# Optimization experiments

Hardware: AMD Instinct MI355X
Metric: run time of the kernel (lower is better)

## Reference

```python
import jax, jax.numpy as jnp
from jax import lax
import numpy as np

DIM = 384
HEADS = 8
MLP_HIDDEN = int(DIM * 4.0)
EPS = 1e-5


def layer_norm(x, g, b):
    m = jnp.mean(x, axis=-1, keepdims=True)
    v = jnp.mean((x - m) ** 2, axis=-1, keepdims=True)
    return (x - m) * lax.rsqrt(v + EPS) * g + b


def conv_pos_enc(x, H, W, w, b):
    # x: (B, N, C) -> depthwise 3x3 conv residual, act=Identity (cpe_act=False)
    B, N, C = x.shape
    feat = jnp.transpose(x, (0, 2, 1)).reshape(B, C, H, W)
    feat = lax.conv_general_dilated(
        feat, w, window_strides=(1, 1), padding='SAME',
        feature_group_count=C, dimension_numbers=('NCHW', 'OIHW', 'NCHW'))
    feat = feat + b[None, :, None, None]
    feat = jnp.transpose(feat.reshape(B, C, N), (0, 2, 1))
    return x + feat


def channel_attn(x, qkv_w, proj_w, proj_b):
    B, N, C = x.shape
    h = HEADS
    hd = C // h
    scale = hd ** (-0.5)
    qkv = x @ qkv_w.T                                # (B, N, 3C)
    qkv = qkv.reshape(B, N, 3, h, hd)
    qkv = jnp.transpose(qkv, (2, 0, 3, 1, 4))        # (3, B, h, N, hd)
    q, k, v = qkv[0], qkv[1], qkv[2]
    k = k * scale
    attn = jnp.einsum('bhnd,bhne->bhde', k, v)       # (B, h, hd, hd)
    attn = jax.nn.softmax(attn, axis=-1)
    out = jnp.einsum('bhde,bhne->bhnd', attn, q)     # (B, h, N, hd)
    out = jnp.transpose(out, (0, 2, 1, 3)).reshape(B, N, C)
    return out @ proj_w.T + proj_b


def mlp(x, fc1_w, fc1_b, fc2_w, fc2_b):
    h = jax.nn.gelu(x @ fc1_w.T + fc1_b, approximate=False)
    return h @ fc2_w.T + fc2_b


def setup_inputs() -> dict:
    key = jax.random.key(0)
    ks = jax.random.split(key, 12)
    C, Hd = DIM, MLP_HIDDEN
    s = 0.02
    return {
        'x': jax.random.normal(ks[0], (32, 784, C), dtype=jnp.float32),
        'H': 28,
        'W': 28,
        'cpe0_w': jax.random.normal(ks[1], (C, 1, 3, 3), dtype=jnp.float32) * s,
        'cpe0_b': jnp.zeros((C,), dtype=jnp.float32),
        'cpe1_w': jax.random.normal(ks[2], (C, 1, 3, 3), dtype=jnp.float32) * s,
        'cpe1_b': jnp.zeros((C,), dtype=jnp.float32),
        'norm1_g': jnp.ones((C,), dtype=jnp.float32),
        'norm1_b': jnp.zeros((C,), dtype=jnp.float32),
        'qkv_w': jax.random.normal(ks[3], (3 * C, C), dtype=jnp.float32) * s,
        'proj_w': jax.random.normal(ks[4], (C, C), dtype=jnp.float32) * s,
        'proj_b': jnp.zeros((C,), dtype=jnp.float32),
        'norm2_g': jnp.ones((C,), dtype=jnp.float32),
        'norm2_b': jnp.zeros((C,), dtype=jnp.float32),
        'fc1_w': jax.random.normal(ks[5], (Hd, C), dtype=jnp.float32) * s,
        'fc1_b': jnp.zeros((Hd,), dtype=jnp.float32),
        'fc2_w': jax.random.normal(ks[6], (C, Hd), dtype=jnp.float32) * s,
        'fc2_b': jnp.zeros((C,), dtype=jnp.float32),
    }


def reference(x, H, W, cpe0_w, cpe0_b, cpe1_w, cpe1_b, norm1_g, norm1_b,
              qkv_w, proj_w, proj_b, norm2_g, norm2_b,
              fc1_w, fc1_b, fc2_w, fc2_b):
    x = conv_pos_enc(x, H, W, cpe0_w, cpe0_b)
    cur = layer_norm(x, norm1_g, norm1_b)
    x = x + channel_attn(cur, qkv_w, proj_w, proj_b)
    x = conv_pos_enc(x, H, W, cpe1_w, cpe1_b)
    x = x + mlp(layer_norm(x, norm2_g, norm2_b), fc1_w, fc1_b, fc2_w, fc2_b)
    return x
```

## Files before the change

### kernel.cpp

```cpp
#include <hip/hip_runtime.h>
#include <hip/hip_bf16.h>
#include <math.h>
#include <stdint.h>

#define B_     32
#define HH_    28
#define WW_    28
#define N_     784
#define C_     384
#define M_     25088
#define HEADS_ 8
#define HD_    48
#define HID_   1536

typedef __bf16 bf16;
typedef __attribute__((ext_vector_type(8))) __bf16 bf16x8;
typedef __attribute__((ext_vector_type(4))) __bf16 bf16x4;
typedef __attribute__((ext_vector_type(4))) float f32x4;

__device__ __forceinline__ void gload_lds16(const void* g, void* l) {
    __builtin_amdgcn_global_load_lds(
        (const __attribute__((address_space(1))) unsigned int*)g,
        (__attribute__((address_space(3))) unsigned int*)(uintptr_t)l,
        16, 0, 0);
}

__device__ __forceinline__ float gelu_f(float v) {
    float u = 0.7978845608028654f * v * (1.f + 0.044715f * v * v);
    return __fdividef(v, 1.f + __expf(-2.f * u));
}

__global__ void convert4_kernel(const float* __restrict__ a, int na,
                                const float* __restrict__ b, int nb,
                                const float* __restrict__ c, int nc,
                                const float* __restrict__ d, int nd,
                                bf16* __restrict__ out) {
    int i = blockIdx.x * 256 + threadIdx.x;
    int j = i;
    const float* src;
    if (j < na) src = a + j;
    else { j -= na;
        if (j < nb) src = b + j;
        else { j -= nb;
            if (j < nc) src = c + j;
            else { j -= nc;
                if (j >= nd) return;
                src = d + j; } } }
    out[i] = (bf16)(*src);
}

__global__ void wtrans_kernel(const float* __restrict__ w0, const float* __restrict__ w1,
                              float* __restrict__ wt0, float* __restrict__ wt1) {
    int i = blockIdx.x * 256 + threadIdx.x;
    if (i >= C_ * 9) return;
    int c = i / 9, t = i - c * 9;
    wt0[t * C_ + c] = w0[i];
    wt1[t * C_ + c] = w1[i];
}

__global__ __launch_bounds__(256)
void cpe_ln_kernel(const float* __restrict__ x, const float* __restrict__ wt,
                   const float* __restrict__ bias, float* __restrict__ y,
                   const float* __restrict__ g, const float* __restrict__ beta,
                   bf16* __restrict__ lnout) {
    const int wave = threadIdx.x >> 6, lane = threadIdx.x & 63;
    const int f = blockIdx.x;
    const int row = (f & 7) * 3136 + (f >> 3) * 4 + wave;
    const int b = row / N_;
    const int n = row - b * N_;
    const int py = n / WW_, px = n - py * WW_;

    float acc[6], ctr[6];
    const float* xrow = x + (size_t)row * C_ + lane;
    #pragma unroll
    for (int j = 0; j < 6; j++) {
        acc[j] = bias[lane + j * 64];
        ctr[j] = xrow[j * 64];
    }

    if (py >= 1 && py <= 26 && px >= 1 && px <= 26) {
        const float* p = x + (size_t)(row - WW_ - 1) * C_ + lane;
        float v[9][6];
        #pragma unroll
        for (int t = 0; t < 9; t++) {
            if (t == 4) continue;
            const float* pt = p + ((t / 3) * WW_ + (t % 3)) * C_;
            #pragma unroll
            for (int j = 0; j < 6; j++) v[t][j] = pt[j * 64];
        }
        #pragma unroll
        for (int t = 0; t < 9; t++) {
            #pragma unroll
            for (int j = 0; j < 6; j++) {
                float xv = (t == 4) ? ctr[j] : v[t][j];
                acc[j] += wt[t * C_ + lane + j * 64] * xv;
            }
        }
    } else {
        #pragma unroll
        for (int t = 0; t < 9; t++) {
            int yy = py + t / 3 - 1, xx = px + t % 3 - 1;
            if (yy < 0 || yy >= HH_ || xx < 0 || xx >= WW_) continue;
            const float* pt = x + (size_t)(b * N_ + yy * WW_ + xx) * C_ + lane;
            #pragma unroll
            for (int j = 0; j < 6; j++)
                acc[j] += wt[t * C_ + lane + j * 64] * pt[j * 64];
        }
    }
    #pragma unroll
    for (int j = 0; j < 6; j++) acc[j] += ctr[j];

    float* yrow = y + (size_t)row * C_ + lane;
    #pragma unroll
    for (int j = 0; j < 6; j++) yrow[j * 64] = acc[j];

    float s = 0.f;
    #pragma unroll
    for (int j = 0; j < 6; j++) s += acc[j];
    #pragma unroll
    for (int off = 1; off < 64; off <<= 1) s += __shfl_xor(s, off, 64);
    float mean = s * (1.f / C_);
    float d[6], vs = 0.f;
    #pragma unroll
    for (int j = 0; j < 6; j++) { d[j] = acc[j] - mean; vs += d[j] * d[j]; }
    #pragma unroll
    for (int off = 1; off < 64; off <<= 1) vs += __shfl_xor(vs, off, 64);
    float rstd = rsqrtf(vs * (1.f / C_) + 1e-5f);
    bf16* lrow = lnout + (size_t)row * C_ + lane;
    #pragma unroll
    for (int j = 0; j < 6; j++) {
        int c = lane + j * 64;
        lrow[j * 64] = (bf16)(d[j] * rstd * g[c] + beta[c]);
    }
}

template<bool BIAS, bool GELU, bool RESID, bool OUTBF>
__global__ __launch_bounds__(256)
void gemm_kernel(const bf16* __restrict__ A, const bf16* __restrict__ Wt,
                 const float* __restrict__ bias, const float* __restrict__ resid,
                 void* __restrict__ outp, int M, int N, int K) {
    __shared__ __align__(16) bf16 As[4 * 4096];
    __shared__ __align__(16) bf16 Bs[4 * 4096];

    const int nbn = gridDim.x, nbm = gridDim.y;
    const int f = blockIdx.y * nbn + blockIdx.x;
    const int grp = f / (8 * nbn);
    const int rem = f - grp * 8 * nbn;
    const int rows = min(8, nbm - grp * 8);
    const int bm = (grp * 8 + rem % rows) * 128;
    const int bn = (rem / rows) * 128;

    const int t = threadIdx.x;
    const int wave = t >> 6, lane = t & 63;
    const int wm = (wave & 1) * 64, wn = (wave >> 1) * 64;
    const int quad = lane >> 4, r = lane & 15;

    const int ldrow = lane >> 2;
    const int ldcol = ((lane & 3) ^ ((lane >> 3) & 3)) * 8;
    const bf16* ga0 = A  + (size_t)(bm + wave * 32 + ldrow) * K + ldcol;
    const bf16* ga1 = ga0 + (size_t)16 * K;
    const bf16* gb0 = Wt + (size_t)(bn + wave * 32 + ldrow) * K + ldcol;
    const bf16* gb1 = gb0 + (size_t)16 * K;
    const int lbase = wave * 1024;

    const int nk = K >> 5;

    auto issue = [&](int st) {
        const int kk = st * 32;
        const int bb = (st & 3) * 4096;
        gload_lds16(ga0 + kk, &As[bb + lbase]);
        gload_lds16(ga1 + kk, &As[bb + lbase + 512]);
        gload_lds16(gb0 + kk, &Bs[bb + lbase]);
        gload_lds16(gb1 + kk, &Bs[bb + lbase + 512]);
    };

    f32x4 acc[4][4] = {};
    issue(0); issue(1); issue(2);

    const int sq = (quad ^ ((r >> 1) & 3)) * 8;

    for (int s = 0; s < nk; ++s) {
        const int left = nk - s;
        if (left >= 3)      asm volatile("s_waitcnt vmcnt(8)" ::: "memory");
        else if (left == 2) asm volatile("s_waitcnt vmcnt(4)" ::: "memory");
        else                asm volatile("s_waitcnt vmcnt(0)" ::: "memory");
        asm volatile("s_barrier" ::: "memory");
        if (s + 3 < nk) issue(s + 3);

        const bf16* as = &As[(s & 3) * 4096];
        const bf16* bs = &Bs[(s & 3) * 4096];
        bf16x8 af[4], bfr[4];
        #pragma unroll
        for (int i = 0; i < 4; i++)
            af[i] = *(const bf16x8*)(&as[(wm + i * 16 + r) * 32 + sq]);
        #pragma unroll
        for (int j = 0; j < 4; j++)
            bfr[j] = *(const bf16x8*)(&bs[(wn + j * 16 + r) * 32 + sq]);
        #pragma unroll
        for (int i = 0; i < 4; i++)
            #pragma unroll
            for (int j = 0; j < 4; j++)
                acc[i][j] = __builtin_amdgcn_mfma_f32_16x16x32_bf16(bfr[j], af[i], acc[i][j], 0, 0, 0);
    }

    #pragma unroll
    for (int j = 0; j < 4; j++) {
        const int n = bn + wn + j * 16 + quad * 4;
        f32x4 bv = {};
        if (BIAS) bv = *(const f32x4*)(&bias[n]);
        #pragma unroll
        for (int i = 0; i < 4; i++) {
            const size_t m = (size_t)(bm + wm + i * 16 + r);
            f32x4 v = acc[i][j];
            if (BIAS) v += bv;
            if (GELU) {
                #pragma unroll
                for (int e = 0; e < 4; e++) v[e] = gelu_f(v[e]);
            }
            if (RESID) v += *(const f32x4*)(&resid[m * N + n]);
            if (OUTBF) {
                bf16x4 ov;
                #pragma unroll
                for (int e = 0; e < 4; e++) ov[e] = (bf16)v[e];
                *(bf16x4*)((bf16*)outp + m * N + n) = ov;
            } else {
                *(f32x4*)((float*)outp + m * N + n) = v;
            }
        }
    }
}

__global__ __launch_bounds__(256)
void attn_fused_kernel(const bf16* __restrict__ qkvb, bf16* __restrict__ outp) {
    __shared__ __align__(16) bf16 stage[4][3872];
    __shared__ float Sred[4][48][49];
    __shared__ __align__(16) bf16 attn_s[48 * 72];

    const int bh = blockIdx.x;
    const int b = bh >> 3, h = bh & 7;
    const int t = threadIdx.x;
    const int wave = t >> 6, lane = t & 63;
    const int quad = lane >> 4, r = lane & 15;
    const int tensor = lane >> 5;
    const int n_local = lane & 31;

    const size_t qkv_base = (size_t)b * N_ * 1152;
    const int toff = 384 + tensor * 384 + h * 48;

    f32x4 acc[3][3] = {};
    bf16* kT = &stage[wave][0];
    bf16* vT = &stage[wave][1936];
    bf16* myT = &stage[wave][tensor * 1936];

    for (int c = wave; c < 25; c += 4) {
        int n0 = c * 32;
        bf16 rowbuf[48];
        if (n0 + n_local < N_) {
            const uint4* src = (const uint4*)(qkvb + qkv_base + (size_t)(n0 + n_local) * 1152 + toff);
            #pragma unroll
            for (int i = 0; i < 6; i++) *(uint4*)(&rowbuf[i * 8]) = src[i];
        } else {
            #pragma unroll
            for (int i = 0; i < 48; i++) rowbuf[i] = (bf16)0.f;
        }
        #pragma unroll
        for (int d = 0; d < 48; d++) myT[d * 40 + n_local] = rowbuf[d];
        bf16x8 af[3], bfv[3];
        #pragma unroll
        for (int i = 0; i < 3; i++) af[i]  = *(const bf16x8*)(&kT[(i * 16 + r) * 40 + quad * 8]);
        #pragma unroll
        for (int j = 0; j < 3; j++) bfv[j] = *(const bf16x8*)(&vT[(j * 16 + r) * 40 + quad * 8]);
        #pragma unroll
        for (int i = 0; i < 3; i++)
            #pragma unroll
            for (int j = 0; j < 3; j++)
                acc[i][j] = __builtin_amdgcn_mfma_f32_16x16x32_bf16(af[i], bfv[j], acc[i][j], 0, 0, 0);
    }

    #pragma unroll
    for (int i = 0; i < 3; i++)
        #pragma unroll
        for (int j = 0; j < 3; j++)
            #pragma unroll
            for (int e = 0; e < 4; e++)
                Sred[wave][i * 16 + quad * 4 + e][j * 16 + r] = acc[i][j][e];
    __syncthreads();

    if (t < 48) {
        float row[48];
        float mx = -1e30f;
        #pragma unroll
        for (int e = 0; e < 48; e++) {
            float s = Sred[0][t][e] + Sred[1][t][e] + Sred[2][t][e] + Sred[3][t][e];
            s *= 0.14433756729740644f;
            row[e] = s;
            mx = fmaxf(mx, s);
        }
        float sum = 0.f;
        #pragma unroll
        for (int e = 0; e < 48; e++) { float ex = __expf(row[e] - mx); row[e] = ex; sum += ex; }
        float inv = 1.f / sum;
        #pragma unroll
        for (int e = 0; e < 48; e++) attn_s[t * 72 + e] = (bf16)(row[e] * inv);
        #pragma unroll
        for (int e = 48; e < 64; e++) attn_s[t * 72 + e] = (bf16)0.f;
    }
    __syncthreads();

    const bf16* qbase = qkvb + qkv_base + h * 48;
    for (int nt = wave; nt < 49; nt += 4) {
        int n0 = nt * 16;
        f32x4 oacc[3] = {};
        #pragma unroll
        for (int kc = 0; kc < 2; kc++) {
            bf16x8 bq = *(const bf16x8*)(qbase + (size_t)(n0 + r) * 1152 + kc * 32 + quad * 8);
            #pragma unroll
            for (int i = 0; i < 3; i++) {
                bf16x8 aa = *(const bf16x8*)(&attn_s[(i * 16 + r) * 72 + kc * 32 + quad * 8]);
                oacc[i] = __builtin_amdgcn_mfma_f32_16x16x32_bf16(aa, bq, oacc[i], 0, 0, 0);
            }
        }
        #pragma unroll
        for (int i = 0; i < 3; i++) {
            bf16x4 ov;
            #pragma unroll
            for (int e = 0; e < 4; e++) ov[e] = (bf16)oacc[i][e];
            *(bf16x4*)(outp + (size_t)(b * N_ + n0 + r) * 384 + h * 48 + i * 16 + quad * 4) = ov;
        }
    }
}

extern "C" void kernel_launch(void* const* d_in, const int* in_sizes, int n_in,
                              void* d_out, int out_size, void* d_ws, size_t ws_size,
                              hipStream_t stream) {
    const float* x      = (const float*)d_in[0];
    const float* cpe0_w = (const float*)d_in[3];
    const float* cpe0_b = (const float*)d_in[4];
    const float* cpe1_w = (const float*)d_in[5];
    const float* cpe1_b = (const float*)d_in[6];
    const float* n1g    = (const float*)d_in[7];
    const float* n1b    = (const float*)d_in[8];
    const float* qkv_w  = (const float*)d_in[9];
    const float* proj_w = (const float*)d_in[10];
    const float* proj_b = (const float*)d_in[11];
    const float* n2g    = (const float*)d_in[12];
    const float* n2b    = (const float*)d_in[13];
    const float* fc1_w  = (const float*)d_in[14];
    const float* fc1_b  = (const float*)d_in[15];
    const float* fc2_w  = (const float*)d_in[16];
    const float* fc2_b  = (const float*)d_in[17];

    char* ws = (char*)d_ws;
    size_t off = 0;
    bf16* cur    = (bf16*)(ws + off); off += (size_t)M_ * C_ * 2;
    bf16* qkvb   = (bf16*)(ws + off);
    float* x3    = (float*)qkvb;
    off += (size_t)M_ * 1152 * 2;
    bf16* hbuf   = (bf16*)(ws + off); off += (size_t)M_ * HID_ * 2;
    bf16* qkv_wb  = (bf16*)(ws + off); off += (size_t)1152 * 384 * 2;
    bf16* proj_wb = (bf16*)(ws + off); off += (size_t)384 * 384 * 2;
    bf16* fc1_wb  = (bf16*)(ws + off); off += (size_t)HID_ * 384 * 2;
    bf16* fc2_wb  = (bf16*)(ws + off); off += (size_t)384 * HID_ * 2;
    float* wt0    = (float*)(ws + off); off += (size_t)C_ * 9 * 4;
    float* wt1    = (float*)(ws + off); off += (size_t)C_ * 9 * 4;
    float* out = (float*)d_out;

    const int na = 442368, nb = 147456, nc = 589824, nd = 589824;
    convert4_kernel<<<(na + nb + nc + nd + 255) / 256, 256, 0, stream>>>(
        qkv_w, na, proj_w, nb, fc1_w, nc, fc2_w, nd, qkv_wb);
    wtrans_kernel<<<(C_ * 9 + 255) / 256, 256, 0, stream>>>(cpe0_w, cpe1_w, wt0, wt1);

    cpe_ln_kernel<<<M_ / 4, 256, 0, stream>>>(x, wt0, cpe0_b, out, n1g, n1b, cur);
    gemm_kernel<false, false, false, true><<<dim3(1152 / 128, M_ / 128), 256, 0, stream>>>(
        cur, qkv_wb, nullptr, nullptr, qkvb, M_, 1152, 384);
    attn_fused_kernel<<<256, 256, 0, stream>>>(qkvb, cur);
    gemm_kernel<true, false, true, false><<<dim3(384 / 128, M_ / 128), 256, 0, stream>>>(
        cur, proj_wb, proj_b, out, out, M_, 384, 384);
    cpe_ln_kernel<<<M_ / 4, 256, 0, stream>>>(out, wt1, cpe1_b, x3, n2g, n2b, cur);
    gemm_kernel<true, true, false, true><<<dim3(HID_ / 128, M_ / 128), 256, 0, stream>>>(
        cur, fc1_wb, fc1_b, nullptr, hbuf, M_, HID_, 384);
    gemm_kernel<true, false, true, false><<<dim3(384 / 128, M_ / 128), 256, 0, stream>>>(
        hbuf, fc2_wb, fc2_b, x3, out, M_, 384, HID_);
}
```

Baseline: 402.8 us.

## Enlarge GEMM tile to 256x128 with 512 threads and 3-stage LDS ring

The GEMM block tile grows from 128x128 to 256x128 and the block from 4 to 8 waves, so each weight tile loaded into LDS is reused across twice as many rows. The LDS pipeline drops from 4 stages to 3 in a single unified buffer. Each wave now loads three 16-row chunks shared across A and B, and the vmcnt waits are adjusted to match. This reduces B-tile traffic and per-block overhead, but the shallower prefetch depth and higher register pressure under launch_bounds(512,4) may limit latency hiding and occupancy.

```diff
diff --git a/kernel.cpp b/kernel.cpp
--- a/kernel.cpp
+++ b/kernel.cpp
@@ -135,60 +135,64 @@
 }
 
 template<bool BIAS, bool GELU, bool RESID, bool OUTBF>
-__global__ __launch_bounds__(256)
+__global__ __launch_bounds__(512, 4)
 void gemm_kernel(const bf16* __restrict__ A, const bf16* __restrict__ Wt,
                  const float* __restrict__ bias, const float* __restrict__ resid,
                  void* __restrict__ outp, int M, int N, int K) {
-    __shared__ __align__(16) bf16 As[4 * 4096];
-    __shared__ __align__(16) bf16 Bs[4 * 4096];
+    __shared__ __align__(16) bf16 S[3 * 12288];
 
     const int nbn = gridDim.x, nbm = gridDim.y;
     const int f = blockIdx.y * nbn + blockIdx.x;
     const int grp = f / (8 * nbn);
     const int rem = f - grp * 8 * nbn;
     const int rows = min(8, nbm - grp * 8);
-    const int bm = (grp * 8 + rem % rows) * 128;
+    const int bm = (grp * 8 + rem % rows) * 256;
     const int bn = (rem / rows) * 128;
 
     const int t = threadIdx.x;
     const int wave = t >> 6, lane = t & 63;
-    const int wm = (wave & 1) * 64, wn = (wave >> 1) * 64;
+    const int wm = (wave >> 1) * 64, wn = (wave & 1) * 64;
     const int quad = lane >> 4, r = lane & 15;
 
     const int ldrow = lane >> 2;
     const int ldcol = ((lane & 3) ^ ((lane >> 3) & 3)) * 8;
-    const bf16* ga0 = A  + (size_t)(bm + wave * 32 + ldrow) * K + ldcol;
-    const bf16* ga1 = ga0 + (size_t)16 * K;
-    const bf16* gb0 = Wt + (size_t)(bn + wave * 32 + ldrow) * K + ldcol;
-    const bf16* gb1 = gb0 + (size_t)16 * K;
-    const int lbase = wave * 1024;
+
+    const bf16 *gp0, *gp1, *gp2;
+    int lo0, lo1, lo2;
+    {
+        const int c0 = 3 * wave;
+        #define CHUNK(c, p, lo) \
+            if ((c) < 16) { p = A + (size_t)(bm + (c) * 16 + ldrow) * K + ldcol; lo = (c) * 512; } \
+            else { p = Wt + (size_t)(bn + ((c) - 16) * 16 + ldrow) * K + ldcol; lo = 8192 + ((c) - 16) * 512; }
+        CHUNK(c0 + 0, gp0, lo0);
+        CHUNK(c0 + 1, gp1, lo1);
+        CHUNK(c0 + 2, gp2, lo2);
+        #undef CHUNK
+    }
 
     const int nk = K >> 5;
 
     auto issue = [&](int st) {
+        const int sb = (st % 3) * 12288;
         const int kk = st * 32;
-        const int bb = (st & 3) * 4096;
-        gload_lds16(ga0 + kk, &As[bb + lbase]);
-        gload_lds16(ga1 + kk, &As[bb + lbase + 512]);
-        gload_lds16(gb0 + kk, &Bs[bb + lbase]);
-        gload_lds16(gb1 + kk, &Bs[bb + lbase + 512]);
+        gload_lds16(gp0 + kk, &S[sb + lo0]);
+        gload_lds16(gp1 + kk, &S[sb + lo1]);
+        gload_lds16(gp2 + kk, &S[sb + lo2]);
     };
 
     f32x4 acc[4][4] = {};
-    issue(0); issue(1); issue(2);
+    issue(0); issue(1);
 
     const int sq = (quad ^ ((r >> 1) & 3)) * 8;
 
     for (int s = 0; s < nk; ++s) {
-        const int left = nk - s;
-        if (left >= 3)      asm volatile("s_waitcnt vmcnt(8)" ::: "memory");
-        else if (left == 2) asm volatile("s_waitcnt vmcnt(4)" ::: "memory");
-        else                asm volatile("s_waitcnt vmcnt(0)" ::: "memory");
+        if (s + 1 < nk) asm volatile("s_waitcnt vmcnt(3)" ::: "memory");
+        else            asm volatile("s_waitcnt vmcnt(0)" ::: "memory");
         asm volatile("s_barrier" ::: "memory");
-        if (s + 3 < nk) issue(s + 3);
-
-        const bf16* as = &As[(s & 3) * 4096];
-        const bf16* bs = &Bs[(s & 3) * 4096];
+        if (s + 2 < nk) issue(s + 2);
+
+        const bf16* as = &S[(s % 3) * 12288];
+        const bf16* bs = as + 8192;
         bf16x8 af[4], bfr[4];
         #pragma unroll
         for (int i = 0; i < 4; i++)
@@ -371,14 +375,14 @@
     wtrans_kernel<<<(C_ * 9 + 255) / 256, 256, 0, stream>>>(cpe0_w, cpe1_w, wt0, wt1);
 
     cpe_ln_kernel<<<M_ / 4, 256, 0, stream>>>(x, wt0, cpe0_b, out, n1g, n1b, cur);
-    gemm_kernel<false, false, false, true><<<dim3(1152 / 128, M_ / 128), 256, 0, stream>>>(
+    gemm_kernel<false, false, false, true><<<dim3(1152 / 128, M_ / 256), 512, 0, stream>>>(
         cur, qkv_wb, nullptr, nullptr, qkvb, M_, 1152, 384);
     attn_fused_kernel<<<256, 256, 0, stream>>>(qkvb, cur);
-    gemm_kernel<true, false, true, false><<<dim3(384 / 128, M_ / 128), 256, 0, stream>>>(
+    gemm_kernel<true, false, true, false><<<dim3(384 / 128, M_ / 256), 512, 0, stream>>>(
         cur, proj_wb, proj_b, out, out, M_, 384, 384);
     cpe_ln_kernel<<<M_ / 4, 256, 0, stream>>>(out, wt1, cpe1_b, x3, n2g, n2b, cur);
-    gemm_kernel<true, true, false, true><<<dim3(HID_ / 128, M_ / 128), 256, 0, stream>>>(
+    gemm_kernel<true, true, false, true><<<dim3(HID_ / 128, M_ / 256), 512, 0, stream>>>(
         cur, fc1_wb, fc1_b, nullptr, hbuf, M_, HID_, 384);
-    gemm_kernel<true, false, true, false><<<dim3(384 / 128, M_ / 128), 256, 0, stream>>>(
+    gemm_kernel<true, false, true, false><<<dim3(384 / 128, M_ / 256), 512, 0, stream>>>(
         hbuf, fc2_wb, fc2_b, x3, out, M_, 384, HID_);
 }
```

Measured after the change: 398.3 us. Within noise of the previous version (-1.1%).

## Restructure GEMM to stage full-K A tile in LDS, stream B from global

Applied to the files above, without the earlier changes.

The GEMM kernel drops its 4-stage pipelined LDS ring for both operands. It now loads a whole 128x384 A block into swizzled LDS in one pass and reads B fragments straight from global memory (through cache) in registers. Blocks grow to 512 threads with 128x192 output tiles, and the launch grids change to match. This removes per-k-step barriers and B staging, at the cost of no overlap between A loads and compute. It also uses a large 96KB LDS tile that limits occupancy, and B reads are uncoalesced and served from global.

```diff
diff --git a/kernel.cpp b/kernel.cpp
--- a/kernel.cpp
+++ b/kernel.cpp
@@ -135,12 +135,11 @@
 }
 
 template<bool BIAS, bool GELU, bool RESID, bool OUTBF>
-__global__ __launch_bounds__(256)
+__global__ __launch_bounds__(512, 2)
 void gemm_kernel(const bf16* __restrict__ A, const bf16* __restrict__ Wt,
                  const float* __restrict__ bias, const float* __restrict__ resid,
                  void* __restrict__ outp, int M, int N, int K) {
-    __shared__ __align__(16) bf16 As[4 * 4096];
-    __shared__ __align__(16) bf16 Bs[4 * 4096];
+    __shared__ __align__(16) bf16 Atile[128 * 384];
 
     const int nbn = gridDim.x, nbm = gridDim.y;
     const int f = blockIdx.y * nbn + blockIdx.x;
@@ -148,63 +147,55 @@
     const int rem = f - grp * 8 * nbn;
     const int rows = min(8, nbm - grp * 8);
     const int bm = (grp * 8 + rem % rows) * 128;
-    const int bn = (rem / rows) * 128;
+    const int bn = (rem / rows) * 192;
 
     const int t = threadIdx.x;
     const int wave = t >> 6, lane = t & 63;
-    const int wm = (wave & 1) * 64, wn = (wave >> 1) * 64;
+    const int wm = (wave & 1) * 64;
+    const int wn = (wave >> 1) * 48;
     const int quad = lane >> 4, r = lane & 15;
 
-    const int ldrow = lane >> 2;
-    const int ldcol = ((lane & 3) ^ ((lane >> 3) & 3)) * 8;
-    const bf16* ga0 = A  + (size_t)(bm + wave * 32 + ldrow) * K + ldcol;
-    const bf16* ga1 = ga0 + (size_t)16 * K;
-    const bf16* gb0 = Wt + (size_t)(bn + wave * 32 + ldrow) * K + ldcol;
-    const bf16* gb1 = gb0 + (size_t)16 * K;
-    const int lbase = wave * 1024;
-
-    const int nk = K >> 5;
-
-    auto issue = [&](int st) {
-        const int kk = st * 32;
-        const int bb = (st & 3) * 4096;
-        gload_lds16(ga0 + kk, &As[bb + lbase]);
-        gload_lds16(ga1 + kk, &As[bb + lbase + 512]);
-        gload_lds16(gb0 + kk, &Bs[bb + lbase]);
-        gload_lds16(gb1 + kk, &Bs[bb + lbase + 512]);
-    };
-
-    f32x4 acc[4][4] = {};
-    issue(0); issue(1); issue(2);
-
-    const int sq = (quad ^ ((r >> 1) & 3)) * 8;
-
-    for (int s = 0; s < nk; ++s) {
-        const int left = nk - s;
-        if (left >= 3)      asm volatile("s_waitcnt vmcnt(8)" ::: "memory");
-        else if (left == 2) asm volatile("s_waitcnt vmcnt(4)" ::: "memory");
-        else                asm volatile("s_waitcnt vmcnt(0)" ::: "memory");
+    const bf16* gB = Wt + (size_t)(bn + wn + r) * K + quad * 8;
+
+    f32x4 acc[4][3] = {};
+
+    for (int ck = 0; ck < K; ck += 384) {
+        if (ck) asm volatile("s_barrier" ::: "memory");
+        #pragma unroll
+        for (int q = 0; q < 12; q++) {
+            const int o = q * 8192 + t * 16;
+            const int row = o / 768;
+            const int kb = o - row * 768;
+            const int slot = (kb >> 4) ^ (row & 7);
+            gload_lds16(A + (size_t)(bm + row) * K + ck + slot * 8,
+                        (char*)Atile + o);
+        }
+        asm volatile("s_waitcnt vmcnt(0)" ::: "memory");
         asm volatile("s_barrier" ::: "memory");
-        if (s + 3 < nk) issue(s + 3);
-
-        const bf16* as = &As[(s & 3) * 4096];
-        const bf16* bs = &Bs[(s & 3) * 4096];
-        bf16x8 af[4], bfr[4];
-        #pragma unroll
-        for (int i = 0; i < 4; i++)
-            af[i] = *(const bf16x8*)(&as[(wm + i * 16 + r) * 32 + sq]);
-        #pragma unroll
-        for (int j = 0; j < 4; j++)
-            bfr[j] = *(const bf16x8*)(&bs[(wn + j * 16 + r) * 32 + sq]);
-        #pragma unroll
-        for (int i = 0; i < 4; i++)
-            #pragma unroll
-            for (int j = 0; j < 4; j++)
-                acc[i][j] = __builtin_amdgcn_mfma_f32_16x16x32_bf16(bfr[j], af[i], acc[i][j], 0, 0, 0);
-    }
-
-    #pragma unroll
-    for (int j = 0; j < 4; j++) {
+
+        #pragma unroll
+        for (int s = 0; s < 12; s++) {
+            bf16x8 af[4], bfr[3];
+            #pragma unroll
+            for (int i = 0; i < 4; i++) {
+                const int row = wm + i * 16 + r;
+                const int kb = (s * 32 + quad * 8) * 2;
+                const int sk = kb ^ ((row & 7) << 4);
+                af[i] = *(const bf16x8*)((const char*)Atile + row * 768 + sk);
+            }
+            #pragma unroll
+            for (int j = 0; j < 3; j++)
+                bfr[j] = *(const bf16x8*)(gB + (size_t)(j * 16) * K + ck + s * 32);
+            #pragma unroll
+            for (int i = 0; i < 4; i++)
+                #pragma unroll
+                for (int j = 0; j < 3; j++)
+                    acc[i][j] = __builtin_amdgcn_mfma_f32_16x16x32_bf16(bfr[j], af[i], acc[i][j], 0, 0, 0);
+        }
+    }
+
+    #pragma unroll
+    for (int j = 0; j < 3; j++) {
         const int n = bn + wn + j * 16 + quad * 4;
         f32x4 bv = {};
         if (BIAS) bv = *(const f32x4*)(&bias[n]);
@@ -371,14 +362,14 @@
     wtrans_kernel<<<(C_ * 9 + 255) / 256, 256, 0, stream>>>(cpe0_w, cpe1_w, wt0, wt1);
 
     cpe_ln_kernel<<<M_ / 4, 256, 0, stream>>>(x, wt0, cpe0_b, out, n1g, n1b, cur);
-    gemm_kernel<false, false, false, true><<<dim3(1152 / 128, M_ / 128), 256, 0, stream>>>(
+    gemm_kernel<false, false, false, true><<<dim3(1152 / 192, M_ / 128), 512, 0, stream>>>(
         cur, qkv_wb, nullptr, nullptr, qkvb, M_, 1152, 384);
     attn_fused_kernel<<<256, 256, 0, stream>>>(qkvb, cur);
-    gemm_kernel<true, false, true, false><<<dim3(384 / 128, M_ / 128), 256, 0, stream>>>(
+    gemm_kernel<true, false, true, false><<<dim3(384 / 192, M_ / 128), 512, 0, stream>>>(
         cur, proj_wb, proj_b, out, out, M_, 384, 384);
     cpe_ln_kernel<<<M_ / 4, 256, 0, stream>>>(out, wt1, cpe1_b, x3, n2g, n2b, cur);
-    gemm_kernel<true, true, false, true><<<dim3(HID_ / 128, M_ / 128), 256, 0, stream>>>(
+    gemm_kernel<true, true, false, true><<<dim3(HID_ / 192, M_ / 128), 512, 0, stream>>>(
         cur, fc1_wb, fc1_b, nullptr, hbuf, M_, HID_, 384);
-    gemm_kernel<true, false, true, false><<<dim3(384 / 128, M_ / 128), 256, 0, stream>>>(
+    gemm_kernel<true, false, true, false><<<dim3(384 / 192, M_ / 128), 512, 0, stream>>>(
         hbuf, fc2_wb, fc2_b, x3, out, M_, 384, HID_);
 }
```

Result: slower. 506.6 us (+25.8%).
